# Optimization experiments

Measured on AMD Instinct MI355X. Metric: run time of the kernel, lower is better.

## Reference

```python
import jax, jax.numpy as jnp
import numpy as np

B, N, VF, EF, DV, DE, LN = 64, 64, 32, 16, 128, 128, 4
EPS_INNER = 128.0  # BatchNorm1d(MAX_N, internal_d_vert): 2nd positional arg is eps (faithful to source bug)
EPS_BN = 1e-5


def gev_layer(v_in, e_in, evW, evb, eW, eb, vW, vb, relu=True):
    act = jax.nn.relu if relu else (lambda x: x)
    ev = v_in @ evW + evb                                   # [B,N,De]
    # outer_v_sum: ev.unsqueeze(1) + ev.unsqueeze(2) -> [B,N,N,De]
    e_out = act(e_in @ eW + eb + ev[:, None, :, :] + ev[:, :, None, :])
    per_v_e = e_out.sum(axis=1)                             # sum-aggregate over dim 1
    v_out = act(jnp.concatenate([per_v_e, v_in], axis=-1) @ vW + vb)
    return v_out, e_out


def bn_flat(v, g, b):
    # BatchNorm1d(N*VF) on [B, N*VF] in training mode (biased var)
    x = v.reshape(-1, N * VF)
    mu = x.mean(axis=0)
    var = x.var(axis=0)
    x = (x - mu) * jax.lax.rsqrt(var + EPS_BN) * g + b
    return x.reshape(-1, N, VF)


def bn_inner(v, g, b):
    # BatchNorm1d(MAX_N, eps=128) on [B, N, D]: channels are the N axis, stats over (B, D)
    mu = v.mean(axis=(0, 2), keepdims=True)
    var = v.var(axis=(0, 2), keepdims=True)
    return (v - mu) * jax.lax.rsqrt(var + EPS_INNER) * g[None, :, None] + b[None, :, None]


def setup_inputs() -> dict:
    key = jax.random.key(0)
    ks = jax.random.split(key, 24)
    s = 0.01  # force_lin_init with init_noise=0.01, biases zero
    nrm = lambda k, shp: jax.random.normal(k, shp, dtype=jnp.float32) * s
    inp = {
        "v": jax.random.normal(ks[0], (B, N, VF), dtype=jnp.float32),
        "e": jax.random.normal(ks[1], (B, N, N, EF), dtype=jnp.float32),
        "bn_in_g": jnp.ones((N * VF,), jnp.float32),
        "bn_in_b": jnp.zeros((N * VF,), jnp.float32),
        "g1_evW": nrm(ks[2], (VF, DE)), "g1_evb": jnp.zeros((DE,), jnp.float32),
        "g1_eW": nrm(ks[3], (EF, DE)), "g1_eb": jnp.zeros((DE,), jnp.float32),
        "g1_vW": nrm(ks[4], (VF + DE, DV)), "g1_vb": jnp.zeros((DV,), jnp.float32),
        "inn_evW": nrm(ks[5], (LN, DV, DE)), "inn_evb": jnp.zeros((LN, DE), jnp.float32),
        "inn_eW": nrm(ks[6], (LN, DE, DE)), "inn_eb": jnp.zeros((LN, DE), jnp.float32),
        "inn_vW": nrm(ks[7], (LN, DV + DE, DV)), "inn_vb": jnp.zeros((LN, DV), jnp.float32),
        "bn_g": jnp.ones((LN, N), jnp.float32),
        "bn_b": jnp.zeros((LN, N), jnp.float32),
        "g3_evW": nrm(ks[8], (DV, 1)), "g3_evb": jnp.zeros((1,), jnp.float32),
        "g3_eW": nrm(ks[9], (DE, 1)), "g3_eb": jnp.zeros((1,), jnp.float32),
        "g3_vW": nrm(ks[10], (DV + 1, 1)), "g3_vb": jnp.zeros((1,), jnp.float32),
    }
    return inp


def reference(v, e, bn_in_g, bn_in_b, g1_evW, g1_evb, g1_eW, g1_eb, g1_vW, g1_vb,
              inn_evW, inn_evb, inn_eW, inn_eb, inn_vW, inn_vb, bn_g, bn_b,
              g3_evW, g3_evb, g3_eW, g3_eb, g3_vW, g3_vb):
    v = bn_flat(v, bn_in_g, bn_in_b)
    v, e = gev_layer(v, e, g1_evW, g1_evb, g1_eW, g1_eb, g1_vW, g1_vb)
    for i in range(LN):
        v_next, e_next = gev_layer(v, e, inn_evW[i], inn_evb[i], inn_eW[i], inn_eb[i], inn_vW[i], inn_vb[i])
        v = v_next + v  # resnet
        e = e_next + e
        v = bn_inner(v, bn_g[i], bn_b[i])
    v, e = gev_layer(v, e, g3_evW, g3_evb, g3_eW, g3_eb, g3_vW, g3_vb, relu=False)
    return v, e
```

## Files before the change

### kernel.cpp

```cpp
#include <hip/hip_runtime.h>
#include <hip/hip_bf16.h>


typedef __bf16 bf16_t;
typedef __bf16 bf16x8 __attribute__((ext_vector_type(8)));
typedef __bf16 bf16x4 __attribute__((ext_vector_type(4)));
typedef float f32x4 __attribute__((ext_vector_type(4)));

__global__ __launch_bounds__(256) void k_bn_in(const float* __restrict__ vin,
    const float* __restrict__ g, const float* __restrict__ bt,
    float* __restrict__ v0) {
  int ch = blockIdx.x * 256 + threadIdx.x;
  float s = 0.f, s2 = 0.f;
  for (int b = 0; b < 64; ++b) { float x = vin[b * 2048 + ch]; s += x; s2 += x * x; }
  float mu = s * (1.f / 64.f);
  float var = s2 * (1.f / 64.f) - mu * mu;
  float sc = rsqrtf(var + 1e-5f) * g[ch];
  float bb = bt[ch];
  for (int b = 0; b < 64; ++b) {
    float x = vin[b * 2048 + ch];
    v0[b * 2048 + ch] = (x - mu) * sc + bb;
  }
}

__global__ __launch_bounds__(256) void k_prep_wt(const float* __restrict__ eW,
    bf16_t* __restrict__ Wt) {
  int idx = blockIdx.x * 256 + threadIdx.x;
  int l = idx >> 14, r = idx & 16383, n = r >> 7, k = r & 127;
  Wt[idx] = (bf16_t)eW[(l << 14) + (k << 7) + n];
}

template <int K>
__global__ __launch_bounds__(128) void k_ev(const float* __restrict__ v_in,
    const float* __restrict__ W, const float* __restrict__ bias,
    float* __restrict__ out) {
  __shared__ float rows[8][K];
  const int r0 = blockIdx.x * 8;
  const int c = threadIdx.x;
  for (int idx = c; idx < 8 * K; idx += 128) {
    int rr = idx / K, kk = idx % K;
    rows[rr][kk] = v_in[(r0 + rr) * K + kk];
  }
  __syncthreads();
  float acc[8];
  const float bv = bias[c];
#pragma unroll
  for (int r = 0; r < 8; ++r) acc[r] = bv;
  for (int k4 = 0; k4 < K; k4 += 4) {
    float w0 = W[(k4 + 0) * 128 + c], w1 = W[(k4 + 1) * 128 + c];
    float w2 = W[(k4 + 2) * 128 + c], w3 = W[(k4 + 3) * 128 + c];
#pragma unroll
    for (int r = 0; r < 8; ++r) {
      float4 x = *(const float4*)&rows[r][k4];
      acc[r] += x.x * w0 + x.y * w1 + x.z * w2 + x.w * w3;
    }
  }
#pragma unroll
  for (int r = 0; r < 8; ++r) out[(r0 + r) * 128 + c] = acc[r];
}

__global__ __launch_bounds__(128) void k_evbn(float* __restrict__ v,
    const float* __restrict__ stats, const float* __restrict__ g,
    const float* __restrict__ bt, const float* __restrict__ W,
    const float* __restrict__ bias, float* __restrict__ out) {
  __shared__ float rows[8][128];
  const int r0 = blockIdx.x * 8;
  const int c = threadIdx.x;
#pragma unroll
  for (int rr = 0; rr < 8; ++rr) {
    int n = (r0 + rr) & 63;
    float mu = stats[n] * (1.f / 8192.f);
    float var = stats[64 + n] * (1.f / 8192.f) - mu * mu;
    float sc = rsqrtf(var + 128.f) * g[n];
    float x = (v[(r0 + rr) * 128 + c] - mu) * sc + bt[n];
    rows[rr][c] = x;
    v[(r0 + rr) * 128 + c] = x;
  }
  __syncthreads();
  float acc[8];
  const float bv = bias[c];
#pragma unroll
  for (int r = 0; r < 8; ++r) acc[r] = bv;
  for (int k4 = 0; k4 < 128; k4 += 4) {
    float w0 = W[(k4 + 0) * 128 + c], w1 = W[(k4 + 1) * 128 + c];
    float w2 = W[(k4 + 2) * 128 + c], w3 = W[(k4 + 3) * 128 + c];
#pragma unroll
    for (int r = 0; r < 8; ++r) {
      float4 x = *(const float4*)&rows[r][k4];
      acc[r] += x.x * w0 + x.y * w1 + x.z * w2 + x.w * w3;
    }
  }
#pragma unroll
  for (int r = 0; r < 8; ++r) out[(r0 + r) * 128 + c] = acc[r];
}

__global__ __launch_bounds__(256) void k_edge_g1(const float* __restrict__ e0,
    const float* __restrict__ eW, const float* __restrict__ eb,
    const float* __restrict__ ev, bf16_t* __restrict__ e_ws,
    float* __restrict__ pve) {
  __shared__ bf16_t A0s[2][64][40];
  __shared__ bf16_t Os[2][64][136];
  const int b = blockIdx.x >> 5, j0 = (blockIdx.x & 31) * 2;
  const int tid = threadIdx.x;
  const int lane = tid & 63, w = tid >> 6;
  const int quad = lane >> 4, l16 = lane & 15;
#pragma unroll
  for (int t = 0; t < 2; ++t) {
    int idx = tid + t * 256;
    int row = idx >> 3, off = (idx & 7) * 4;
    int jc = off >> 4, k = off & 15;
    f32x4 x = *(const f32x4*)&e0[((b * 64 + row) * 64 + j0) * 16 + off];
    bf16x4 y;
#pragma unroll
    for (int r = 0; r < 4; ++r) y[r] = (bf16_t)x[r];
    *(bf16x4*)&A0s[jc][row][k] = y;
    bf16x4 z = {(bf16_t)0.f, (bf16_t)0.f, (bf16_t)0.f, (bf16_t)0.f};
    *(bf16x4*)&A0s[jc][row][16 + k] = z;
  }
  const int c0[2] = {w * 32 + quad * 4, w * 32 + 16 + quad * 4};
  bf16x8 wf[2];
#pragma unroll
  for (int nt = 0; nt < 2; ++nt) {
    const int c = w * 32 + nt * 16 + l16;
#pragma unroll
    for (int jj = 0; jj < 8; ++jj)
      wf[nt][jj] = (quad < 2) ? (bf16_t)eW[(quad * 8 + jj) * 128 + c] : (bf16_t)0.f;
  }
  f32x4 acc[2][4][2];
  {
    f32x4 ebv[2], evj[2][2], evi[4][2];
#pragma unroll
    for (int nt = 0; nt < 2; ++nt) {
      ebv[nt] = *(const f32x4*)&eb[c0[nt]];
#pragma unroll
      for (int jc = 0; jc < 2; ++jc)
        evj[jc][nt] = *(const f32x4*)&ev[(b * 64 + j0 + jc) * 128 + c0[nt]];
#pragma unroll
      for (int mt = 0; mt < 4; ++mt)
        evi[mt][nt] = *(const f32x4*)&ev[(b * 64 + mt * 16 + l16) * 128 + c0[nt]];
    }
#pragma unroll
    for (int jc = 0; jc < 2; ++jc)
#pragma unroll
      for (int mt = 0; mt < 4; ++mt)
#pragma unroll
        for (int nt = 0; nt < 2; ++nt)
          acc[jc][mt][nt] = ebv[nt] + evj[jc][nt] + evi[mt][nt];
  }
  __syncthreads();
#pragma unroll
  for (int jc = 0; jc < 2; ++jc) {
#pragma unroll
    for (int mt = 0; mt < 4; ++mt) {
      bf16x8 ef = *(const bf16x8*)&A0s[jc][mt * 16 + l16][quad * 8];
#pragma unroll
      for (int nt = 0; nt < 2; ++nt)
        acc[jc][mt][nt] = __builtin_amdgcn_mfma_f32_16x16x32_bf16(wf[nt], ef, acc[jc][mt][nt], 0, 0, 0);
    }
  }
#pragma unroll
  for (int jc = 0; jc < 2; ++jc) {
#pragma unroll
    for (int nt = 0; nt < 2; ++nt) {
      f32x4 ps = {0.f, 0.f, 0.f, 0.f};
#pragma unroll
      for (int mt = 0; mt < 4; ++mt) {
        const int i = mt * 16 + l16;
        bf16x4 outv;
#pragma unroll
        for (int r = 0; r < 4; ++r) {
          float vv = fmaxf(acc[jc][mt][nt][r], 0.f);
          ps[r] += vv;
          outv[r] = (bf16_t)vv;
        }
        *(bf16x4*)&Os[jc][i][c0[nt]] = outv;
      }
#pragma unroll
      for (int m = 1; m <= 8; m <<= 1) {
#pragma unroll
        for (int r = 0; r < 4; ++r) ps[r] += __shfl_xor(ps[r], m);
      }
      if (l16 == 0) *(f32x4*)&pve[(b * 64 + j0 + jc) * 128 + c0[nt]] = ps;
    }
  }
  __syncthreads();
#pragma unroll
  for (int t = 0; t < 8; ++t) {
    int idx = tid + t * 256;
    int row = idx >> 5, off = (idx & 31) * 8;
    int jc = off >> 7, c = off & 127;
    *(int4*)&e_ws[((b * 64 + row) * 64 + j0) * 128 + off] = *(const int4*)&Os[jc][row][c];
  }
}

__global__ __launch_bounds__(128) void k_v_g1(const float* __restrict__ pve,
    const float* __restrict__ v0, const float* __restrict__ vW,
    const float* __restrict__ vb, float* __restrict__ v) {
  __shared__ float in[8][160];
  const int r0 = blockIdx.x * 8;
  const int c = threadIdx.x;
#pragma unroll
  for (int t = 0; t < 8; ++t) {
    int idx = c + t * 128;
    int rr = idx >> 7, k = idx & 127;
    in[rr][k] = pve[(r0 + rr) * 128 + k];
  }
#pragma unroll
  for (int t = 0; t < 2; ++t) {
    int idx = c + t * 128;
    int rr = idx >> 5, k = idx & 31;
    in[rr][128 + k] = v0[(r0 + rr) * 32 + k];
  }
  __syncthreads();
  float acc[8];
  const float bv = vb[c];
#pragma unroll
  for (int r = 0; r < 8; ++r) acc[r] = bv;
  for (int k4 = 0; k4 < 160; k4 += 4) {
    float w0 = vW[(k4 + 0) * 128 + c], w1 = vW[(k4 + 1) * 128 + c];
    float w2 = vW[(k4 + 2) * 128 + c], w3 = vW[(k4 + 3) * 128 + c];
#pragma unroll
    for (int r = 0; r < 8; ++r) {
      float4 x = *(const float4*)&in[r][k4];
      acc[r] += x.x * w0 + x.y * w1 + x.z * w2 + x.w * w3;
    }
  }
#pragma unroll
  for (int r = 0; r < 8; ++r) v[(r0 + r) * 128 + c] = fmaxf(acc[r], 0.f);
}

__global__ __launch_bounds__(256) void k_edge_inner(bf16_t* __restrict__ e_ws,
    const bf16_t* __restrict__ Wt, const float* __restrict__ eb,
    const float* __restrict__ ev, float* __restrict__ pve) {
  __shared__ bf16_t As[2][64][136];
  const int b = blockIdx.x >> 5, j0 = (blockIdx.x & 31) * 2;
  const int tid = threadIdx.x;
  const int lane = tid & 63, w = tid >> 6;
  const int quad = lane >> 4, l16 = lane & 15;
  int4 stg[8];
#pragma unroll
  for (int t = 0; t < 8; ++t) {
    int idx = tid + t * 256;
    int row = idx >> 5, off = (idx & 31) * 8;
    stg[t] = *(const int4*)&e_ws[((b * 64 + row) * 64 + j0) * 128 + off];
  }
  bf16x8 wf[2][4];
#pragma unroll
  for (int nt = 0; nt < 2; ++nt)
#pragma unroll
    for (int ks = 0; ks < 4; ++ks)
      wf[nt][ks] = *(const bf16x8*)&Wt[(w * 32 + nt * 16 + l16) * 128 + ks * 32 + quad * 8];
  const int c0[2] = {w * 32 + quad * 4, w * 32 + 16 + quad * 4};
  f32x4 acc[2][4][2];
  {
    f32x4 ebv[2], evj[2][2], evi[4][2];
#pragma unroll
    for (int nt = 0; nt < 2; ++nt) {
      ebv[nt] = *(const f32x4*)&eb[c0[nt]];
#pragma unroll
      for (int jc = 0; jc < 2; ++jc)
        evj[jc][nt] = *(const f32x4*)&ev[(b * 64 + j0 + jc) * 128 + c0[nt]];
#pragma unroll
      for (int mt = 0; mt < 4; ++mt)
        evi[mt][nt] = *(const f32x4*)&ev[(b * 64 + mt * 16 + l16) * 128 + c0[nt]];
    }
#pragma unroll
    for (int jc = 0; jc < 2; ++jc)
#pragma unroll
      for (int mt = 0; mt < 4; ++mt)
#pragma unroll
        for (int nt = 0; nt < 2; ++nt)
          acc[jc][mt][nt] = ebv[nt] + evj[jc][nt] + evi[mt][nt];
  }
#pragma unroll
  for (int t = 0; t < 8; ++t) {
    int idx = tid + t * 256;
    int row = idx >> 5, off = (idx & 31) * 8;
    *(int4*)&As[off >> 7][row][off & 127] = stg[t];
  }
  __syncthreads();
#pragma unroll
  for (int ks = 0; ks < 4; ++ks) {
    bf16x8 ef[2][4];
#pragma unroll
    for (int jc = 0; jc < 2; ++jc)
#pragma unroll
      for (int mt = 0; mt < 4; ++mt)
        ef[jc][mt] = *(const bf16x8*)&As[jc][mt * 16 + l16][ks * 32 + quad * 8];
#pragma unroll
    for (int jc = 0; jc < 2; ++jc)
#pragma unroll
      for (int mt = 0; mt < 4; ++mt)
#pragma unroll
        for (int nt = 0; nt < 2; ++nt)
          acc[jc][mt][nt] = __builtin_amdgcn_mfma_f32_16x16x32_bf16(wf[nt][ks], ef[jc][mt], acc[jc][mt][nt], 0, 0, 0);
  }
  __syncthreads();
#pragma unroll
  for (int jc = 0; jc < 2; ++jc) {
#pragma unroll
    for (int nt = 0; nt < 2; ++nt) {
      f32x4 ps = {0.f, 0.f, 0.f, 0.f};
#pragma unroll
      for (int mt = 0; mt < 4; ++mt) {
        const int i = mt * 16 + l16;
        bf16x4 eo = *(const bf16x4*)&As[jc][i][c0[nt]];
        bf16x4 outv;
#pragma unroll
        for (int r = 0; r < 4; ++r) {
          float vv = fmaxf(acc[jc][mt][nt][r], 0.f);
          ps[r] += vv;
          outv[r] = (bf16_t)(vv + (float)eo[r]);
        }
        *(bf16x4*)&As[jc][i][c0[nt]] = outv;
      }
#pragma unroll
      for (int m = 1; m <= 8; m <<= 1) {
#pragma unroll
        for (int r = 0; r < 4; ++r) ps[r] += __shfl_xor(ps[r], m);
      }
      if (l16 == 0) *(f32x4*)&pve[(b * 64 + j0 + jc) * 128 + c0[nt]] = ps;
    }
  }
  __syncthreads();
#pragma unroll
  for (int t = 0; t < 8; ++t) {
    int idx = tid + t * 256;
    int row = idx >> 5, off = (idx & 31) * 8;
    *(int4*)&e_ws[((b * 64 + row) * 64 + j0) * 128 + off] = *(const int4*)&As[off >> 7][row][off & 127];
  }
}

__global__ __launch_bounds__(128) void k_v_inner(const float* __restrict__ pve,
    float* __restrict__ v, const float* __restrict__ vW,
    const float* __restrict__ vb, float* __restrict__ stats) {
  __shared__ float in[8][256];
  __shared__ float outs[8][132];
  const int r0 = blockIdx.x * 8;
  const int c = threadIdx.x;
#pragma unroll
  for (int t = 0; t < 8; ++t) {
    int idx = c + t * 128;
    int rr = idx >> 7, k = idx & 127;
    in[rr][k] = pve[(r0 + rr) * 128 + k];
    in[rr][128 + k] = v[(r0 + rr) * 128 + k];
  }
  __syncthreads();
  float acc[8];
  const float bv = vb[c];
#pragma unroll
  for (int r = 0; r < 8; ++r) acc[r] = bv;
  for (int k4 = 0; k4 < 256; k4 += 4) {
    float w0 = vW[(k4 + 0) * 128 + c], w1 = vW[(k4 + 1) * 128 + c];
    float w2 = vW[(k4 + 2) * 128 + c], w3 = vW[(k4 + 3) * 128 + c];
#pragma unroll
    for (int r = 0; r < 8; ++r) {
      float4 x = *(const float4*)&in[r][k4];
      acc[r] += x.x * w0 + x.y * w1 + x.z * w2 + x.w * w3;
    }
  }
#pragma unroll
  for (int r = 0; r < 8; ++r) {
    float val = fmaxf(acc[r], 0.f) + in[r][128 + c];
    outs[r][c] = val;
    v[(r0 + r) * 128 + c] = val;
  }
  __syncthreads();
  if (c < 8) {
    float s = 0.f, s2 = 0.f;
    for (int k = 0; k < 128; ++k) { float x = outs[c][k]; s += x; s2 += x * x; }
    int n = (r0 + c) & 63;
    atomicAdd(&stats[n], s);
    atomicAdd(&stats[64 + n], s2);
  }
}

__global__ __launch_bounds__(256) void k_bn_apply(float* __restrict__ v,
    const float* __restrict__ stats, const float* __restrict__ g,
    const float* __restrict__ bt) {
  int idx = blockIdx.x * 256 + threadIdx.x;
  int n = (idx >> 7) & 63;
  float mu = stats[n] * (1.f / 8192.f);
  float var = stats[64 + n] * (1.f / 8192.f) - mu * mu;
  float sc = rsqrtf(var + 128.f) * g[n];
  v[idx] = (v[idx] - mu) * sc + bt[n];
}

__global__ __launch_bounds__(256) void k_ev3(const float* __restrict__ v,
    const float* __restrict__ W, const float* __restrict__ bias,
    float* __restrict__ ev3) {
  int r = blockIdx.x * 4 + (threadIdx.x >> 6);
  int lane = threadIdx.x & 63;
  float acc = v[r * 128 + lane] * W[lane] + v[r * 128 + 64 + lane] * W[64 + lane];
#pragma unroll
  for (int m = 1; m < 64; m <<= 1) acc += __shfl_xor(acc, m);
  if (lane == 0) ev3[r] = acc + bias[0];
}

__global__ __launch_bounds__(256) void k_edge_g3(const bf16_t* __restrict__ e_ws,
    const float* __restrict__ eW3, const float* __restrict__ eb3,
    const float* __restrict__ ev3, float* __restrict__ out_e,
    float* __restrict__ pve3) {
  __shared__ float W3[128];
  const int b = blockIdx.x >> 6, i = blockIdx.x & 63;
  const int tid = threadIdx.x;
  if (tid < 128) W3[tid] = eW3[tid];
  __syncthreads();
  const int j = tid >> 2, cs = (tid & 3) * 32;
  const bf16_t* ep = &e_ws[(size_t)((b * 64 + i) * 64 + j) * 128 + cs];
  float acc = 0.f;
#pragma unroll
  for (int t = 0; t < 4; ++t) {
    bf16x8 x = *(const bf16x8*)&ep[t * 8];
#pragma unroll
    for (int u = 0; u < 8; ++u) acc += (float)x[u] * W3[cs + t * 8 + u];
  }
  acc += __shfl_xor(acc, 1);
  acc += __shfl_xor(acc, 2);
  if ((tid & 3) == 0) {
    float s = acc + eb3[0] + ev3[b * 64 + i] + ev3[b * 64 + j];
    out_e[(b * 64 + i) * 64 + j] = s;
    atomicAdd(&pve3[b * 64 + j], s);
  }
}

__global__ __launch_bounds__(256) void k_v_g3(const float* __restrict__ v,
    const float* __restrict__ pve3, const float* __restrict__ vW,
    const float* __restrict__ vb, float* __restrict__ out_v) {
  int r = blockIdx.x * 4 + (threadIdx.x >> 6);
  int lane = threadIdx.x & 63;
  float acc = v[r * 128 + lane] * vW[1 + lane] + v[r * 128 + 64 + lane] * vW[65 + lane];
#pragma unroll
  for (int m = 1; m < 64; m <<= 1) acc += __shfl_xor(acc, m);
  if (lane == 0) out_v[r] = acc + pve3[r] * vW[0] + vb[0];
}

extern "C" void kernel_launch(void* const* d_in, const int* in_sizes, int n_in,
                              void* d_out, int out_size, void* d_ws, size_t ws_size,
                              hipStream_t stream) {
  const float* in_v    = (const float*)d_in[0];
  const float* in_e    = (const float*)d_in[1];
  const float* bn_in_g = (const float*)d_in[2];
  const float* bn_in_b = (const float*)d_in[3];
  const float* g1_evW  = (const float*)d_in[4];
  const float* g1_evb  = (const float*)d_in[5];
  const float* g1_eW   = (const float*)d_in[6];
  const float* g1_eb   = (const float*)d_in[7];
  const float* g1_vW   = (const float*)d_in[8];
  const float* g1_vb   = (const float*)d_in[9];
  const float* inn_evW = (const float*)d_in[10];
  const float* inn_evb = (const float*)d_in[11];
  const float* inn_eW  = (const float*)d_in[12];
  const float* inn_eb  = (const float*)d_in[13];
  const float* inn_vW  = (const float*)d_in[14];
  const float* inn_vb  = (const float*)d_in[15];
  const float* bn_g    = (const float*)d_in[16];
  const float* bn_b    = (const float*)d_in[17];
  const float* g3_evW  = (const float*)d_in[18];
  const float* g3_evb  = (const float*)d_in[19];
  const float* g3_eW   = (const float*)d_in[20];
  const float* g3_eb   = (const float*)d_in[21];
  const float* g3_vW   = (const float*)d_in[22];
  const float* g3_vb   = (const float*)d_in[23];

  char* ws = (char*)d_ws;
  bf16_t* e_ws = (bf16_t*)(ws);
  float* v     = (float*)(ws + 67108864);
  float* ev    = (float*)(ws + 69206016);
  float* pve   = (float*)(ws + 71303168);
  float* v0    = (float*)(ws + 73400320);
  bf16_t* Wt   = (bf16_t*)(ws + 73924608);
  float* ev3   = (float*)(ws + 74055680);
  float* pve3  = (float*)(ws + 74072064);
  float* stats = (float*)(ws + 74088448);

  float* out_v = (float*)d_out;
  float* out_e = (float*)d_out + 4096;

  hipMemsetAsync(pve3, 0, 16384 + 2048, stream);
  k_bn_in<<<8, 256, 0, stream>>>(in_v, bn_in_g, bn_in_b, v0);
  k_prep_wt<<<256, 256, 0, stream>>>(inn_eW, Wt);

  k_ev<32><<<512, 128, 0, stream>>>(v0, g1_evW, g1_evb, ev);
  k_edge_g1<<<2048, 256, 0, stream>>>(in_e, g1_eW, g1_eb, ev, e_ws, pve);
  k_v_g1<<<512, 128, 0, stream>>>(pve, v0, g1_vW, g1_vb, v);

  for (int l = 0; l < 4; ++l) {
    if (l == 0)
      k_ev<128><<<512, 128, 0, stream>>>(v, inn_evW, inn_evb, ev);
    else
      k_evbn<<<512, 128, 0, stream>>>(v, stats + (l - 1) * 128, bn_g + (l - 1) * 64,
                                      bn_b + (l - 1) * 64, inn_evW + l * 16384,
                                      inn_evb + l * 128, ev);
    k_edge_inner<<<2048, 256, 0, stream>>>(e_ws, Wt + l * 16384, inn_eb + l * 128, ev, pve);
    k_v_inner<<<512, 128, 0, stream>>>(pve, v, inn_vW + l * 32768, inn_vb + l * 128,
                                       stats + l * 128);
  }
  k_bn_apply<<<2048, 256, 0, stream>>>(v, stats + 3 * 128, bn_g + 192, bn_b + 192);

  k_ev3<<<1024, 256, 0, stream>>>(v, g3_evW, g3_evb, ev3);
  k_edge_g3<<<4096, 256, 0, stream>>>(e_ws, g3_eW, g3_eb, ev3, out_e, pve3);
  k_v_g3<<<1024, 256, 0, stream>>>(v, pve3, g3_vW, g3_vb, out_v);
}
```

Before: 422.0 us.

## Pipeline edge-inner over four columns and fuse final BN, ev3, and prep kernels

k_edge_inner now handles four j columns per block, double-buffered in LDS, so the next column's global loads are issued while MFMA runs on the current one. The grid shrinks to 1024 blocks. The memset and the two setup kernels are merged into one k_prep launch. The final BN apply and the ev3 kernel are folded into k_edge_g3 and k_v_g3, which recompute the normalization and ev3 per block. This removes several launches and one pass over v, but k_edge_g3 now redundantly renormalizes 64 rows of v in every one of its 4096 blocks.

```diff
diff --git a/kernel.cpp b/kernel.cpp
--- a/kernel.cpp
+++ b/kernel.cpp
@@ -7,27 +7,35 @@
 typedef __bf16 bf16x4 __attribute__((ext_vector_type(4)));
 typedef float f32x4 __attribute__((ext_vector_type(4)));
 
-__global__ __launch_bounds__(256) void k_bn_in(const float* __restrict__ vin,
+__device__ __forceinline__ void bar_lgkm() {
+  asm volatile("s_waitcnt lgkmcnt(0)\n\ts_barrier" ::: "memory");
+}
+
+__global__ __launch_bounds__(256) void k_prep(const float* __restrict__ vin,
     const float* __restrict__ g, const float* __restrict__ bt,
-    float* __restrict__ v0) {
-  int ch = blockIdx.x * 256 + threadIdx.x;
-  float s = 0.f, s2 = 0.f;
-  for (int b = 0; b < 64; ++b) { float x = vin[b * 2048 + ch]; s += x; s2 += x * x; }
-  float mu = s * (1.f / 64.f);
-  float var = s2 * (1.f / 64.f) - mu * mu;
-  float sc = rsqrtf(var + 1e-5f) * g[ch];
-  float bb = bt[ch];
-  for (int b = 0; b < 64; ++b) {
-    float x = vin[b * 2048 + ch];
-    v0[b * 2048 + ch] = (x - mu) * sc + bb;
-  }
-}
-
-__global__ __launch_bounds__(256) void k_prep_wt(const float* __restrict__ eW,
-    bf16_t* __restrict__ Wt) {
-  int idx = blockIdx.x * 256 + threadIdx.x;
-  int l = idx >> 14, r = idx & 16383, n = r >> 7, k = r & 127;
-  Wt[idx] = (bf16_t)eW[(l << 14) + (k << 7) + n];
+    const float* __restrict__ eW, float* __restrict__ v0,
+    bf16_t* __restrict__ Wt, float* __restrict__ pve3, float* __restrict__ stats) {
+  const int blk = blockIdx.x, tid = threadIdx.x;
+  if (blk < 8) {
+    int ch = blk * 256 + tid;
+    float s = 0.f, s2 = 0.f;
+    for (int b = 0; b < 64; ++b) { float x = vin[b * 2048 + ch]; s += x; s2 += x * x; }
+    float mu = s * (1.f / 64.f);
+    float var = s2 * (1.f / 64.f) - mu * mu;
+    float sc = rsqrtf(var + 1e-5f) * g[ch];
+    float bb = bt[ch];
+    for (int b = 0; b < 64; ++b) {
+      float x = vin[b * 2048 + ch];
+      v0[b * 2048 + ch] = (x - mu) * sc + bb;
+    }
+  } else if (blk < 264) {
+    int idx = (blk - 8) * 256 + tid;
+    int l = idx >> 14, r = idx & 16383, n = r >> 7, k = r & 127;
+    Wt[idx] = (bf16_t)eW[(l << 14) + (k << 7) + n];
+  } else {
+    for (int i = tid; i < 4096; i += 256) pve3[i] = 0.f;
+    for (int i = tid; i < 512; i += 256) stats[i] = 0.f;
+  }
 }
 
 template <int K>
@@ -233,101 +241,116 @@
     const bf16_t* __restrict__ Wt, const float* __restrict__ eb,
     const float* __restrict__ ev, float* __restrict__ pve) {
   __shared__ bf16_t As[2][64][136];
-  const int b = blockIdx.x >> 5, j0 = (blockIdx.x & 31) * 2;
   const int tid = threadIdx.x;
   const int lane = tid & 63, w = tid >> 6;
   const int quad = lane >> 4, l16 = lane & 15;
-  int4 stg[8];
-#pragma unroll
-  for (int t = 0; t < 8; ++t) {
-    int idx = tid + t * 256;
-    int row = idx >> 5, off = (idx & 31) * 8;
-    stg[t] = *(const int4*)&e_ws[((b * 64 + row) * 64 + j0) * 128 + off];
-  }
+  const int b = blockIdx.x >> 4;
+  const int jb = (blockIdx.x & 15) * 4;
+  const int c0[2] = {w * 32 + quad * 4, w * 32 + 16 + quad * 4};
   bf16x8 wf[2][4];
 #pragma unroll
   for (int nt = 0; nt < 2; ++nt)
 #pragma unroll
     for (int ks = 0; ks < 4; ++ks)
       wf[nt][ks] = *(const bf16x8*)&Wt[(w * 32 + nt * 16 + l16) * 128 + ks * 32 + quad * 8];
-  const int c0[2] = {w * 32 + quad * 4, w * 32 + 16 + quad * 4};
-  f32x4 acc[2][4][2];
-  {
-    f32x4 ebv[2], evj[2][2], evi[4][2];
-#pragma unroll
-    for (int nt = 0; nt < 2; ++nt) {
-      ebv[nt] = *(const f32x4*)&eb[c0[nt]];
-#pragma unroll
-      for (int jc = 0; jc < 2; ++jc)
-        evj[jc][nt] = *(const f32x4*)&ev[(b * 64 + j0 + jc) * 128 + c0[nt]];
+  f32x4 ebv[2], evi[4][2];
+#pragma unroll
+  for (int nt = 0; nt < 2; ++nt) {
+    ebv[nt] = *(const f32x4*)&eb[c0[nt]];
+#pragma unroll
+    for (int mt = 0; mt < 4; ++mt)
+      evi[mt][nt] = *(const f32x4*)&ev[(b * 64 + mt * 16 + l16) * 128 + c0[nt]];
+  }
+  int4 stg[4];
+  f32x4 evj[2];
+#pragma unroll
+  for (int u = 0; u < 4; ++u) {
+    int idx = tid + u * 256;
+    stg[u] = *(const int4*)&e_ws[((b * 64 + (idx >> 4)) * 64 + jb) * 128 + (idx & 15) * 8];
+  }
+#pragma unroll
+  for (int nt = 0; nt < 2; ++nt)
+    evj[nt] = *(const f32x4*)&ev[(b * 64 + jb) * 128 + c0[nt]];
+#pragma unroll
+  for (int u = 0; u < 4; ++u) {
+    int idx = tid + u * 256;
+    *(int4*)&As[0][idx >> 4][(idx & 15) * 8] = stg[u];
+  }
+  bar_lgkm();
+#pragma unroll
+  for (int t = 0; t < 4; ++t) {
+    const int X = t & 1, j = jb + t;
+    int4 stg2[4];
+    f32x4 evj2[2];
+    if (t < 3) {
+#pragma unroll
+      for (int u = 0; u < 4; ++u) {
+        int idx = tid + u * 256;
+        stg2[u] = *(const int4*)&e_ws[((b * 64 + (idx >> 4)) * 64 + (j + 1)) * 128 + (idx & 15) * 8];
+      }
+#pragma unroll
+      for (int nt = 0; nt < 2; ++nt)
+        evj2[nt] = *(const f32x4*)&ev[(b * 64 + j + 1) * 128 + c0[nt]];
+    }
+    f32x4 acc[4][2];
+#pragma unroll
+    for (int mt = 0; mt < 4; ++mt)
+#pragma unroll
+      for (int nt = 0; nt < 2; ++nt)
+        acc[mt][nt] = ebv[nt] + evj[nt] + evi[mt][nt];
+#pragma unroll
+    for (int ks = 0; ks < 4; ++ks) {
+      bf16x8 ef[4];
 #pragma unroll
       for (int mt = 0; mt < 4; ++mt)
-        evi[mt][nt] = *(const f32x4*)&ev[(b * 64 + mt * 16 + l16) * 128 + c0[nt]];
-    }
-#pragma unroll
-    for (int jc = 0; jc < 2; ++jc)
+        ef[mt] = *(const bf16x8*)&As[X][mt * 16 + l16][ks * 32 + quad * 8];
 #pragma unroll
       for (int mt = 0; mt < 4; ++mt)
 #pragma unroll
         for (int nt = 0; nt < 2; ++nt)
-          acc[jc][mt][nt] = ebv[nt] + evj[jc][nt] + evi[mt][nt];
-  }
-#pragma unroll
-  for (int t = 0; t < 8; ++t) {
-    int idx = tid + t * 256;
-    int row = idx >> 5, off = (idx & 31) * 8;
-    *(int4*)&As[off >> 7][row][off & 127] = stg[t];
-  }
-  __syncthreads();
-#pragma unroll
-  for (int ks = 0; ks < 4; ++ks) {
-    bf16x8 ef[2][4];
-#pragma unroll
-    for (int jc = 0; jc < 2; ++jc)
-#pragma unroll
-      for (int mt = 0; mt < 4; ++mt)
-        ef[jc][mt] = *(const bf16x8*)&As[jc][mt * 16 + l16][ks * 32 + quad * 8];
-#pragma unroll
-    for (int jc = 0; jc < 2; ++jc)
-#pragma unroll
-      for (int mt = 0; mt < 4; ++mt)
-#pragma unroll
-        for (int nt = 0; nt < 2; ++nt)
-          acc[jc][mt][nt] = __builtin_amdgcn_mfma_f32_16x16x32_bf16(wf[nt][ks], ef[jc][mt], acc[jc][mt][nt], 0, 0, 0);
-  }
-  __syncthreads();
-#pragma unroll
-  for (int jc = 0; jc < 2; ++jc) {
+          acc[mt][nt] = __builtin_amdgcn_mfma_f32_16x16x32_bf16(wf[nt][ks], ef[mt], acc[mt][nt], 0, 0, 0);
+    }
+    bar_lgkm();
 #pragma unroll
     for (int nt = 0; nt < 2; ++nt) {
       f32x4 ps = {0.f, 0.f, 0.f, 0.f};
 #pragma unroll
       for (int mt = 0; mt < 4; ++mt) {
         const int i = mt * 16 + l16;
-        bf16x4 eo = *(const bf16x4*)&As[jc][i][c0[nt]];
+        bf16x4 eo = *(const bf16x4*)&As[X][i][c0[nt]];
         bf16x4 outv;
 #pragma unroll
         for (int r = 0; r < 4; ++r) {
-          float vv = fmaxf(acc[jc][mt][nt][r], 0.f);
+          float vv = fmaxf(acc[mt][nt][r], 0.f);
           ps[r] += vv;
           outv[r] = (bf16_t)(vv + (float)eo[r]);
         }
-        *(bf16x4*)&As[jc][i][c0[nt]] = outv;
+        *(bf16x4*)&As[X][i][c0[nt]] = outv;
       }
 #pragma unroll
       for (int m = 1; m <= 8; m <<= 1) {
 #pragma unroll
         for (int r = 0; r < 4; ++r) ps[r] += __shfl_xor(ps[r], m);
       }
-      if (l16 == 0) *(f32x4*)&pve[(b * 64 + j0 + jc) * 128 + c0[nt]] = ps;
-    }
-  }
-  __syncthreads();
-#pragma unroll
-  for (int t = 0; t < 8; ++t) {
-    int idx = tid + t * 256;
-    int row = idx >> 5, off = (idx & 31) * 8;
-    *(int4*)&e_ws[((b * 64 + row) * 64 + j0) * 128 + off] = *(const int4*)&As[off >> 7][row][off & 127];
+      if (l16 == 0) *(f32x4*)&pve[(b * 64 + j) * 128 + c0[nt]] = ps;
+    }
+    bar_lgkm();
+#pragma unroll
+    for (int u = 0; u < 4; ++u) {
+      int idx = tid + u * 256;
+      *(int4*)&e_ws[((b * 64 + (idx >> 4)) * 64 + j) * 128 + (idx & 15) * 8] =
+          *(const int4*)&As[X][idx >> 4][(idx & 15) * 8];
+    }
+    if (t < 3) {
+#pragma unroll
+      for (int u = 0; u < 4; ++u) {
+        int idx = tid + u * 256;
+        *(int4*)&As[1 - X][idx >> 4][(idx & 15) * 8] = stg2[u];
+      }
+      evj[0] = evj2[0];
+      evj[1] = evj2[1];
+    }
+    bar_lgkm();
   }
 }
 
@@ -375,61 +398,82 @@
   }
 }
 
-__global__ __launch_bounds__(256) void k_bn_apply(float* __restrict__ v,
-    const float* __restrict__ stats, const float* __restrict__ g,
-    const float* __restrict__ bt) {
-  int idx = blockIdx.x * 256 + threadIdx.x;
-  int n = (idx >> 7) & 63;
-  float mu = stats[n] * (1.f / 8192.f);
-  float var = stats[64 + n] * (1.f / 8192.f) - mu * mu;
-  float sc = rsqrtf(var + 128.f) * g[n];
-  v[idx] = (v[idx] - mu) * sc + bt[n];
-}
-
-__global__ __launch_bounds__(256) void k_ev3(const float* __restrict__ v,
-    const float* __restrict__ W, const float* __restrict__ bias,
-    float* __restrict__ ev3) {
+__global__ __launch_bounds__(256) void k_edge_g3(const bf16_t* __restrict__ e_ws,
+    const float* __restrict__ vv, const float* __restrict__ stats3,
+    const float* __restrict__ g, const float* __restrict__ bt,
+    const float* __restrict__ evW3, const float* __restrict__ evb3,
+    const float* __restrict__ eW3, const float* __restrict__ eb3,
+    float* __restrict__ out_e, float* __restrict__ pve3) {
+  __shared__ float vbn[64][132];
+  __shared__ float scs[64], shs[64];
+  __shared__ float W3e[128], W3ee[128];
+  __shared__ float ev3s[64];
+  const int b = blockIdx.x >> 6, i = blockIdx.x & 63;
+  const int tid = threadIdx.x;
+  if (tid < 64) {
+    float mu = stats3[tid] * (1.f / 8192.f);
+    float var = stats3[64 + tid] * (1.f / 8192.f) - mu * mu;
+    float sc = rsqrtf(var + 128.f) * g[tid];
+    scs[tid] = sc;
+    shs[tid] = bt[tid] - mu * sc;
+  }
+  if (tid < 128) W3ee[tid] = eW3[tid];
+  else W3e[tid - 128] = evW3[tid - 128];
+  __syncthreads();
+#pragma unroll
+  for (int t = 0; t < 8; ++t) {
+    int idx = t * 1024 + tid * 4;
+    int row = idx >> 7, c = idx & 127;
+    f32x4 x = *(const f32x4*)&vv[(b * 64 + row) * 128 + c];
+    f32x4 y = x * scs[row] + shs[row];
+    *(f32x4*)&vbn[row][c] = y;
+  }
+  __syncthreads();
+  {
+    int r = tid >> 2, q = tid & 3;
+    float a = 0.f;
+#pragma unroll
+    for (int u = 0; u < 32; ++u) a += vbn[r][q * 32 + u] * W3e[q * 32 + u];
+    a += __shfl_xor(a, 1);
+    a += __shfl_xor(a, 2);
+    if (q == 0) ev3s[r] = a + evb3[0];
+  }
+  __syncthreads();
+  {
+    const int j = tid >> 2, cs = (tid & 3) * 32;
+    const bf16_t* ep = &e_ws[(size_t)((b * 64 + i) * 64 + j) * 128 + cs];
+    float acc = 0.f;
+#pragma unroll
+    for (int t = 0; t < 4; ++t) {
+      bf16x8 x = *(const bf16x8*)&ep[t * 8];
+#pragma unroll
+      for (int u = 0; u < 8; ++u) acc += (float)x[u] * W3ee[cs + t * 8 + u];
+    }
+    acc += __shfl_xor(acc, 1);
+    acc += __shfl_xor(acc, 2);
+    if ((tid & 3) == 0) {
+      float s = acc + eb3[0] + ev3s[i] + ev3s[j];
+      out_e[(b * 64 + i) * 64 + j] = s;
+      atomicAdd(&pve3[b * 64 + j], s);
+    }
+  }
+}
+
+__global__ __launch_bounds__(256) void k_v_g3(const float* __restrict__ vv,
+    const float* __restrict__ stats3, const float* __restrict__ g,
+    const float* __restrict__ bt, const float* __restrict__ pve3,
+    const float* __restrict__ vW, const float* __restrict__ vb,
+    float* __restrict__ out_v) {
   int r = blockIdx.x * 4 + (threadIdx.x >> 6);
   int lane = threadIdx.x & 63;
-  float acc = v[r * 128 + lane] * W[lane] + v[r * 128 + 64 + lane] * W[64 + lane];
-#pragma unroll
-  for (int m = 1; m < 64; m <<= 1) acc += __shfl_xor(acc, m);
-  if (lane == 0) ev3[r] = acc + bias[0];
-}
-
-__global__ __launch_bounds__(256) void k_edge_g3(const bf16_t* __restrict__ e_ws,
-    const float* __restrict__ eW3, const float* __restrict__ eb3,
-    const float* __restrict__ ev3, float* __restrict__ out_e,
-    float* __restrict__ pve3) {
-  __shared__ float W3[128];
-  const int b = blockIdx.x >> 6, i = blockIdx.x & 63;
-  const int tid = threadIdx.x;
-  if (tid < 128) W3[tid] = eW3[tid];
-  __syncthreads();
-  const int j = tid >> 2, cs = (tid & 3) * 32;
-  const bf16_t* ep = &e_ws[(size_t)((b * 64 + i) * 64 + j) * 128 + cs];
-  float acc = 0.f;
-#pragma unroll
-  for (int t = 0; t < 4; ++t) {
-    bf16x8 x = *(const bf16x8*)&ep[t * 8];
-#pragma unroll
-    for (int u = 0; u < 8; ++u) acc += (float)x[u] * W3[cs + t * 8 + u];
-  }
-  acc += __shfl_xor(acc, 1);
-  acc += __shfl_xor(acc, 2);
-  if ((tid & 3) == 0) {
-    float s = acc + eb3[0] + ev3[b * 64 + i] + ev3[b * 64 + j];
-    out_e[(b * 64 + i) * 64 + j] = s;
-    atomicAdd(&pve3[b * 64 + j], s);
-  }
-}
-
-__global__ __launch_bounds__(256) void k_v_g3(const float* __restrict__ v,
-    const float* __restrict__ pve3, const float* __restrict__ vW,
-    const float* __restrict__ vb, float* __restrict__ out_v) {
-  int r = blockIdx.x * 4 + (threadIdx.x >> 6);
-  int lane = threadIdx.x & 63;
-  float acc = v[r * 128 + lane] * vW[1 + lane] + v[r * 128 + 64 + lane] * vW[65 + lane];
+  int n = r & 63;
+  float mu = stats3[n] * (1.f / 8192.f);
+  float var = stats3[64 + n] * (1.f / 8192.f) - mu * mu;
+  float sc = rsqrtf(var + 128.f) * g[n];
+  float sh = bt[n] - mu * sc;
+  float x1 = vv[r * 128 + lane] * sc + sh;
+  float x2 = vv[r * 128 + 64 + lane] * sc + sh;
+  float acc = x1 * vW[1 + lane] + x2 * vW[65 + lane];
 #pragma unroll
   for (int m = 1; m < 64; m <<= 1) acc += __shfl_xor(acc, m);
   if (lane == 0) out_v[r] = acc + pve3[r] * vW[0] + vb[0];
@@ -470,16 +514,13 @@
   float* pve   = (float*)(ws + 71303168);
   float* v0    = (float*)(ws + 73400320);
   bf16_t* Wt   = (bf16_t*)(ws + 73924608);
-  float* ev3   = (float*)(ws + 74055680);
   float* pve3  = (float*)(ws + 74072064);
   float* stats = (float*)(ws + 74088448);
 
   float* out_v = (float*)d_out;
   float* out_e = (float*)d_out + 4096;
 
-  hipMemsetAsync(pve3, 0, 16384 + 2048, stream);
-  k_bn_in<<<8, 256, 0, stream>>>(in_v, bn_in_g, bn_in_b, v0);
-  k_prep_wt<<<256, 256, 0, stream>>>(inn_eW, Wt);
+  k_prep<<<265, 256, 0, stream>>>(in_v, bn_in_g, bn_in_b, inn_eW, v0, Wt, pve3, stats);
 
   k_ev<32><<<512, 128, 0, stream>>>(v0, g1_evW, g1_evb, ev);
   k_edge_g1<<<2048, 256, 0, stream>>>(in_e, g1_eW, g1_eb, ev, e_ws, pve);
@@ -492,13 +533,13 @@
       k_evbn<<<512, 128, 0, stream>>>(v, stats + (l - 1) * 128, bn_g + (l - 1) * 64,
                                       bn_b + (l - 1) * 64, inn_evW + l * 16384,
                                       inn_evb + l * 128, ev);
-    k_edge_inner<<<2048, 256, 0, stream>>>(e_ws, Wt + l * 16384, inn_eb + l * 128, ev, pve);
+    k_edge_inner<<<1024, 256, 0, stream>>>(e_ws, Wt + l * 16384, inn_eb + l * 128, ev, pve);
     k_v_inner<<<512, 128, 0, stream>>>(pve, v, inn_vW + l * 32768, inn_vb + l * 128,
                                        stats + l * 128);
   }
-  k_bn_apply<<<2048, 256, 0, stream>>>(v, stats + 3 * 128, bn_g + 192, bn_b + 192);
-
-  k_ev3<<<1024, 256, 0, stream>>>(v, g3_evW, g3_evb, ev3);
-  k_edge_g3<<<4096, 256, 0, stream>>>(e_ws, g3_eW, g3_eb, ev3, out_e, pve3);
-  k_v_g3<<<1024, 256, 0, stream>>>(v, pve3, g3_vW, g3_vb, out_v);
-}
+
+  k_edge_g3<<<4096, 256, 0, stream>>>(e_ws, v, stats + 384, bn_g + 192, bn_b + 192,
+                                      g3_evW, g3_evb, g3_eW, g3_eb, out_e, pve3);
+  k_v_g3<<<1024, 256, 0, stream>>>(v, stats + 384, bn_g + 192, bn_b + 192, pve3,
+                                   g3_vW, g3_vb, out_v);
+}
```

Result: slower. 457.1 us (+8.3%).
